# Performance work log

Hardware: AMD Instinct MI355X
Metric: run time of the kernel (lower is better)

Reference implementation:

```python
import jax, jax.numpy as jnp
import numpy as np

N_NODES = 100000
N_EDGES = 1600000
D_IN = 256
D_OUT = 128


def setup_inputs() -> dict:
    key = jax.random.key(0)
    k1, k2, k3, k4, k5, k6 = jax.random.split(key, 6)
    inp = {
        "input": jax.random.normal(k1, (N_NODES, D_IN), dtype=jnp.float32),
        "edge_row": jax.random.randint(k2, (N_EDGES,), 0, N_NODES),
        "edge_col": jax.random.randint(k3, (N_EDGES,), 0, N_NODES),
        "edge_val": jax.random.uniform(k4, (N_EDGES,), dtype=jnp.float32),
        "W": jax.random.normal(k5, (D_IN, D_OUT), dtype=jnp.float32) * (1.0 / np.sqrt(D_IN)),
        "b": jax.random.normal(k6, (D_OUT,), dtype=jnp.float32) * 0.01,
    }
    return inp


def reference(input, edge_row, edge_col, edge_val, W, b):
    # support = Linear(input)  -> [N, D_OUT]
    support = jnp.dot(input, W) + b
    # sparse.mm(adj, support): out[r] = sum_e val[e] * support[col[e]] for edges with row[e]==r
    msgs = edge_val[:, None] * support[edge_col]  # [E, D_OUT]
    agg = jax.ops.segment_sum(msgs, edge_row, num_segments=N_NODES)  # [N, D_OUT]
    return jnp.tanh(agg)
```

## Files before the change

kernel.cpp:

```cpp
#include <hip/hip_runtime.h>
#include <math.h>

#define N_NODES 100000
#define N_EDGES 1600000
#define D_IN 256
#define D_OUT 128

#define OFF_SUPPORT 0
#define OFF_COUNTS  51200000
#define OFF_CSREV   51600008
#define OFF_BSUMS   64400008
#define OFF_WTHI    64400416
#define OFF_WTLO    64465952

#define SCAN_CHUNK  1024
#define SCAN_BLOCKS ((N_NODES + SCAN_CHUNK - 1) / SCAN_CHUNK)

#define GB 128
#define GEMM_BLOCKS (((N_NODES + GB - 1) / GB) * 2)
#define EDGE_BLOCKS ((N_EDGES + 255) / 256)

typedef __attribute__((ext_vector_type(8))) short s8v;
typedef __attribute__((ext_vector_type(4))) float f4v;

__device__ __forceinline__ short f2bf(float x) {
  unsigned u = __float_as_uint(x);
  unsigned r = u + 0x7FFF + ((u >> 16) & 1);
  return (short)(r >> 16);
}
__device__ __forceinline__ float bf2f(short h) {
  return __uint_as_float(((unsigned)(unsigned short)h) << 16);
}

__device__ __forceinline__ void cvt8(float4 a, float4 b, s8v& h, s8v& l) {
  float f[8] = {a.x, a.y, a.z, a.w, b.x, b.y, b.z, b.w};
#pragma unroll
  for (int i = 0; i < 8; i++) {
    short hh = f2bf(f[i]);
    h[i] = hh;
    l[i] = f2bf(f[i] - bf2f(hh));
  }
}

typedef const float __attribute__((address_space(1)))* gas1f;
typedef float __attribute__((address_space(3)))* las3f;
__device__ __forceinline__ void gload_lds16(const float* g, float* l) {
  __builtin_amdgcn_global_load_lds((gas1f)g, (las3f)l, 16, 0, 0);
}

__global__ __launch_bounds__(256) void wconv_kernel(
    const float* __restrict__ W, short* __restrict__ wt_hi,
    short* __restrict__ wt_lo) {
  int idx = blockIdx.x * 256 + threadIdx.x;
  int k = idx >> 7;
  int n = idx & 127;
  float v = W[idx];
  short h = f2bf(v);
  wt_hi[n * 256 + k] = h;
  wt_lo[n * 256 + k] = f2bf(v - bf2f(h));
}

__device__ __forceinline__ void gemm_body(
    int gb, const float* __restrict__ input, const short* __restrict__ wt_hi,
    const short* __restrict__ wt_lo, const float* __restrict__ b,
    float* __restrict__ support) {
  __shared__ float Af[4][2][32][32];
  const int t = threadIdx.x;
  const int lane = t & 63;
  const int wv = t >> 6;
  const int qm = lane & 15;
  const int quad = lane >> 4;
  const int tile_m = gb >> 1;
  const int ch = gb & 1;
  const int node0 = tile_m * GB;
  const int col0 = ch * 64;

  const int srow = lane >> 3;
  const int gc = (lane & 7) ^ srow;

  auto stage = [&](int kt, int buf) {
#pragma unroll
    for (int j = 0; j < 4; ++j) {
      int nd = node0 + wv * 32 + j * 8 + srow;
      if (nd > N_NODES - 1) nd = N_NODES - 1;
      gload_lds16(input + (size_t)nd * D_IN + kt * 32 + gc * 4,
                  &Af[wv][buf][j * 8][0]);
    }
  };

  stage(0, 0);

  f4v acc[2][4];
#pragma unroll
  for (int mt = 0; mt < 2; mt++)
#pragma unroll
    for (int nt = 0; nt < 4; nt++) acc[mt][nt] = (f4v){0.f, 0.f, 0.f, 0.f};

  const int p0 = (2 * quad) ^ (qm & 7);
  const int p1 = (2 * quad + 1) ^ (qm & 7);

#pragma unroll
  for (int kt = 0; kt < 8; ++kt) {
    const int cb = kt & 1;
    asm volatile("s_waitcnt vmcnt(0)" ::: "memory");
    float4 x00 = *(const float4*)&Af[wv][cb][qm][p0 * 4];
    float4 x01 = *(const float4*)&Af[wv][cb][qm][p1 * 4];
    float4 x10 = *(const float4*)&Af[wv][cb][qm + 16][p0 * 4];
    float4 x11 = *(const float4*)&Af[wv][cb][qm + 16][p1 * 4];

    const int koff = kt * 32 + quad * 8;
    s8v bh[4], bl[4];
#pragma unroll
    for (int nt = 0; nt < 4; ++nt) {
      size_t bo = (size_t)(col0 + nt * 16 + qm) * 256 + koff;
      bh[nt] = *(const s8v*)(wt_hi + bo);
      bl[nt] = *(const s8v*)(wt_lo + bo);
    }
    __builtin_amdgcn_sched_barrier(0);
    if (kt < 7) stage(kt + 1, cb ^ 1);
    __builtin_amdgcn_sched_barrier(0);

    s8v ah0, al0, ah1, al1;
    cvt8(x00, x01, ah0, al0);
    cvt8(x10, x11, ah1, al1);
#pragma unroll
    for (int nt = 0; nt < 4; ++nt) {
      acc[0][nt] = __builtin_amdgcn_mfma_f32_16x16x32_bf16(ah0, bh[nt], acc[0][nt], 0, 0, 0);
      acc[0][nt] = __builtin_amdgcn_mfma_f32_16x16x32_bf16(ah0, bl[nt], acc[0][nt], 0, 0, 0);
      acc[0][nt] = __builtin_amdgcn_mfma_f32_16x16x32_bf16(al0, bh[nt], acc[0][nt], 0, 0, 0);
      acc[1][nt] = __builtin_amdgcn_mfma_f32_16x16x32_bf16(ah1, bh[nt], acc[1][nt], 0, 0, 0);
      acc[1][nt] = __builtin_amdgcn_mfma_f32_16x16x32_bf16(ah1, bl[nt], acc[1][nt], 0, 0, 0);
      acc[1][nt] = __builtin_amdgcn_mfma_f32_16x16x32_bf16(al1, bh[nt], acc[1][nt], 0, 0, 0);
    }
  }

  float bias[4];
#pragma unroll
  for (int nt = 0; nt < 4; nt++) bias[nt] = b[col0 + nt * 16 + qm];
#pragma unroll
  for (int mt = 0; mt < 2; mt++) {
#pragma unroll
    for (int nt = 0; nt < 4; nt++) {
      int col = col0 + nt * 16 + qm;
#pragma unroll
      for (int r = 0; r < 4; r++) {
        int node = node0 + wv * 32 + mt * 16 + quad * 4 + r;
        if (node < N_NODES)
          support[(size_t)node * D_OUT + col] = acc[mt][nt][r] + bias[nt];
      }
    }
  }
}

__global__ __launch_bounds__(256, 4) void gemm_hist_kernel(
    const float* __restrict__ input, const short* __restrict__ wt_hi,
    const short* __restrict__ wt_lo, const float* __restrict__ b,
    float* __restrict__ support, const int* __restrict__ erow,
    int* __restrict__ counts, int* __restrict__ pos_e) {
  if (blockIdx.x < GEMM_BLOCKS) {
    gemm_body(blockIdx.x, input, wt_hi, wt_lo, b, support);
  } else {
    int e = (blockIdx.x - GEMM_BLOCKS) * 256 + threadIdx.x;
    if (e < N_EDGES) pos_e[e] = atomicAdd(&counts[erow[e]], 1);
  }
}

__global__ __launch_bounds__(256) void build_kernel(
    const int* __restrict__ erow, const int* __restrict__ ecol,
    const float* __restrict__ eval, const int* __restrict__ offsets,
    const int* __restrict__ pos_e, int2* __restrict__ csr_ev) {
  int e = blockIdx.x * 256 + threadIdx.x;
  if (e < N_EDGES) {
    int idx = offsets[erow[e]] + pos_e[e];
    csr_ev[idx] = make_int2(ecol[e], __float_as_int(eval[e]));
  }
}

__global__ __launch_bounds__(256) void scan_phase1(const int* __restrict__ counts,
                                                   int* __restrict__ bsums) {
  __shared__ int ts[256];
  int t = threadIdx.x;
  int idx0 = blockIdx.x * SCAN_CHUNK + t * 4;
  int s = 0;
#pragma unroll
  for (int i = 0; i < 4; i++)
    if (idx0 + i < N_NODES) s += counts[idx0 + i];
  ts[t] = s;
  __syncthreads();
#pragma unroll
  for (int off = 128; off > 0; off >>= 1) {
    if (t < off) ts[t] += ts[t + off];
    __syncthreads();
  }
  if (t == 0) bsums[blockIdx.x] = ts[0];
}

__global__ __launch_bounds__(128) void scan_phase2(int* __restrict__ bsums) {
  __shared__ int s[128];
  int t = threadIdx.x;
  int v = (t < SCAN_BLOCKS) ? bsums[t] : 0;
  s[t] = v;
  __syncthreads();
#pragma unroll
  for (int off = 1; off < 128; off <<= 1) {
    int x = (t >= off) ? s[t - off] : 0;
    __syncthreads();
    s[t] += x;
    __syncthreads();
  }
  if (t < SCAN_BLOCKS) bsums[t] = s[t] - v;
}

__global__ __launch_bounds__(256) void scan_phase3(int* __restrict__ counts,
                                                   const int* __restrict__ bsums) {
  __shared__ int ts[256];
  int t = threadIdx.x;
  int b = blockIdx.x;
  int idx0 = b * SCAN_CHUNK + t * 4;
  int v[4];
  int s = 0;
#pragma unroll
  for (int i = 0; i < 4; i++) {
    v[i] = (idx0 + i < N_NODES) ? counts[idx0 + i] : 0;
    s += v[i];
  }
  ts[t] = s;
  __syncthreads();
#pragma unroll
  for (int off = 1; off < 256; off <<= 1) {
    int x = (t >= off) ? ts[t - off] : 0;
    __syncthreads();
    ts[t] += x;
    __syncthreads();
  }
  int run = bsums[b] + ts[t] - s;
#pragma unroll
  for (int i = 0; i < 4; i++) {
    int idx = idx0 + i;
    if (idx < N_NODES) counts[idx] = run;
    run += v[i];
  }
  if (b == 0 && t == 0) counts[N_NODES] = N_EDGES;
}

__global__ __launch_bounds__(256) void agg_kernel(
    const int* __restrict__ offsets, const int2* __restrict__ csr_ev,
    const float* __restrict__ support, float* __restrict__ out) {
  int r = blockIdx.x * 8 + (threadIdx.x >> 5);
  int l4 = (threadIdx.x & 31) * 4;
  int beg = offsets[r];
  int end = offsets[r + 1];
  float4 acc = make_float4(0.f, 0.f, 0.f, 0.f);
  int j = beg;
  for (; j + 8 <= end; j += 8) {
    int2 e[8];
    float4 s[8];
#pragma unroll
    for (int u = 0; u < 8; u++) e[u] = csr_ev[j + u];
#pragma unroll
    for (int u = 0; u < 8; u++)
      s[u] = *(const float4*)(support + (size_t)e[u].x * D_OUT + l4);
#pragma unroll
    for (int u = 0; u < 8; u++) {
      float v = __int_as_float(e[u].y);
      acc.x = fmaf(v, s[u].x, acc.x);
      acc.y = fmaf(v, s[u].y, acc.y);
      acc.z = fmaf(v, s[u].z, acc.z);
      acc.w = fmaf(v, s[u].w, acc.w);
    }
  }
  for (; j < end; j++) {
    int2 ev = csr_ev[j];
    float4 s = *(const float4*)(support + (size_t)ev.x * D_OUT + l4);
    float v = __int_as_float(ev.y);
    acc.x = fmaf(v, s.x, acc.x);
    acc.y = fmaf(v, s.y, acc.y);
    acc.z = fmaf(v, s.z, acc.z);
    acc.w = fmaf(v, s.w, acc.w);
  }
  *(float4*)(out + (size_t)r * D_OUT + l4) =
      make_float4(tanhf(acc.x), tanhf(acc.y), tanhf(acc.z), tanhf(acc.w));
}

extern "C" void kernel_launch(void* const* d_in, const int* in_sizes, int n_in,
                              void* d_out, int out_size, void* d_ws, size_t ws_size,
                              hipStream_t stream) {
  const float* input = (const float*)d_in[0];
  const int* erow = (const int*)d_in[1];
  const int* ecol = (const int*)d_in[2];
  const float* eval = (const float*)d_in[3];
  const float* W = (const float*)d_in[4];
  const float* b = (const float*)d_in[5];
  float* out = (float*)d_out;

  char* ws = (char*)d_ws;
  float* support = (float*)(ws + OFF_SUPPORT);
  int* counts = (int*)(ws + OFF_COUNTS);
  int2* csr_ev = (int2*)(ws + OFF_CSREV);
  int* bsums = (int*)(ws + OFF_BSUMS);
  short* wt_hi = (short*)(ws + OFF_WTHI);
  short* wt_lo = (short*)(ws + OFF_WTLO);
  int* pos_e = (int*)d_out;

  hipLaunchKernelGGL(wconv_kernel, dim3((D_IN * D_OUT) / 256), dim3(256), 0,
                     stream, W, wt_hi, wt_lo);
  hipMemsetAsync(ws + OFF_COUNTS, 0, (size_t)(N_NODES + 1) * 4, stream);

  hipLaunchKernelGGL(gemm_hist_kernel, dim3(GEMM_BLOCKS + EDGE_BLOCKS),
                     dim3(256), 0, stream, input, wt_hi, wt_lo, b, support,
                     erow, counts, pos_e);
  hipLaunchKernelGGL(scan_phase1, dim3(SCAN_BLOCKS), dim3(256), 0, stream,
                     counts, bsums);
  hipLaunchKernelGGL(scan_phase2, dim3(1), dim3(128), 0, stream, bsums);
  hipLaunchKernelGGL(scan_phase3, dim3(SCAN_BLOCKS), dim3(256), 0, stream,
                     counts, bsums);
  hipLaunchKernelGGL(build_kernel, dim3(EDGE_BLOCKS), dim3(256), 0, stream,
                     erow, ecol, eval, counts, pos_e, csr_ev);
  hipLaunchKernelGGL(agg_kernel, dim3(N_NODES / 8), dim3(256), 0, stream,
                     counts, csr_ev, support, out);
}
```

Measured before the change: 457.2 us.

## Split GEMM from histogram, widen GEMM tile to all columns, deepen prefetch

Each GEMM block now computes all 128 output columns for its 128 rows, so each input tile is read once instead of twice. The A-tile staging becomes two stages deep with a partial vmcnt wait, so loads stay in flight across iterations. The fused GEMM+histogram kernel is split into separate hist and gemm launches, which gives up the overlap of atomics with GEMM work. Doubling the accumulators and B registers raises register pressure, and launch bounds drop from 4 to 2 blocks per CU.

```diff
diff --git a/kernel.cpp b/kernel.cpp
--- a/kernel.cpp
+++ b/kernel.cpp
@@ -17,7 +17,7 @@
 #define SCAN_BLOCKS ((N_NODES + SCAN_CHUNK - 1) / SCAN_CHUNK)
 
 #define GB 128
-#define GEMM_BLOCKS (((N_NODES + GB - 1) / GB) * 2)
+#define GEMM_BLOCKS ((N_NODES + GB - 1) / GB)
 #define EDGE_BLOCKS ((N_EDGES + 255) / 256)
 
 typedef __attribute__((ext_vector_type(8))) short s8v;
@@ -60,20 +60,18 @@
   wt_lo[n * 256 + k] = f2bf(v - bf2f(h));
 }
 
-__device__ __forceinline__ void gemm_body(
-    int gb, const float* __restrict__ input, const short* __restrict__ wt_hi,
+__global__ __launch_bounds__(256, 2) void gemm_kernel(
+    const float* __restrict__ input, const short* __restrict__ wt_hi,
     const short* __restrict__ wt_lo, const float* __restrict__ b,
     float* __restrict__ support) {
   __shared__ float Af[4][2][32][32];
+  const int gb = blockIdx.x;
   const int t = threadIdx.x;
   const int lane = t & 63;
   const int wv = t >> 6;
   const int qm = lane & 15;
   const int quad = lane >> 4;
-  const int tile_m = gb >> 1;
-  const int ch = gb & 1;
-  const int node0 = tile_m * GB;
-  const int col0 = ch * 64;
+  const int node0 = gb * GB;
 
   const int srow = lane >> 3;
   const int gc = (lane & 7) ^ srow;
@@ -89,12 +87,13 @@
   };
 
   stage(0, 0);
-
-  f4v acc[2][4];
+  stage(1, 1);
+
+  f4v acc[2][8];
 #pragma unroll
   for (int mt = 0; mt < 2; mt++)
 #pragma unroll
-    for (int nt = 0; nt < 4; nt++) acc[mt][nt] = (f4v){0.f, 0.f, 0.f, 0.f};
+    for (int nt = 0; nt < 8; nt++) acc[mt][nt] = (f4v){0.f, 0.f, 0.f, 0.f};
 
   const int p0 = (2 * quad) ^ (qm & 7);
   const int p1 = (2 * quad + 1) ^ (qm & 7);
@@ -102,29 +101,31 @@
 #pragma unroll
   for (int kt = 0; kt < 8; ++kt) {
     const int cb = kt & 1;
-    asm volatile("s_waitcnt vmcnt(0)" ::: "memory");
+    asm volatile("s_waitcnt vmcnt(4)" ::: "memory");
     float4 x00 = *(const float4*)&Af[wv][cb][qm][p0 * 4];
     float4 x01 = *(const float4*)&Af[wv][cb][qm][p1 * 4];
     float4 x10 = *(const float4*)&Af[wv][cb][qm + 16][p0 * 4];
     float4 x11 = *(const float4*)&Af[wv][cb][qm + 16][p1 * 4];
+    asm volatile("s_waitcnt lgkmcnt(0)" ::: "memory");
+    __builtin_amdgcn_sched_barrier(0);
 
     const int koff = kt * 32 + quad * 8;
-    s8v bh[4], bl[4];
-#pragma unroll
-    for (int nt = 0; nt < 4; ++nt) {
-      size_t bo = (size_t)(col0 + nt * 16 + qm) * 256 + koff;
+    s8v bh[8], bl[8];
+#pragma unroll
+    for (int nt = 0; nt < 8; ++nt) {
+      size_t bo = (size_t)(nt * 16 + qm) * 256 + koff;
       bh[nt] = *(const s8v*)(wt_hi + bo);
       bl[nt] = *(const s8v*)(wt_lo + bo);
     }
     __builtin_amdgcn_sched_barrier(0);
-    if (kt < 7) stage(kt + 1, cb ^ 1);
+    if (kt < 6) stage(kt + 2, cb);
     __builtin_amdgcn_sched_barrier(0);
 
     s8v ah0, al0, ah1, al1;
     cvt8(x00, x01, ah0, al0);
     cvt8(x10, x11, ah1, al1);
 #pragma unroll
-    for (int nt = 0; nt < 4; ++nt) {
+    for (int nt = 0; nt < 8; ++nt) {
       acc[0][nt] = __builtin_amdgcn_mfma_f32_16x16x32_bf16(ah0, bh[nt], acc[0][nt], 0, 0, 0);
       acc[0][nt] = __builtin_amdgcn_mfma_f32_16x16x32_bf16(ah0, bl[nt], acc[0][nt], 0, 0, 0);
       acc[0][nt] = __builtin_amdgcn_mfma_f32_16x16x32_bf16(al0, bh[nt], acc[0][nt], 0, 0, 0);
@@ -134,14 +135,14 @@
     }
   }
 
-  float bias[4];
-#pragma unroll
-  for (int nt = 0; nt < 4; nt++) bias[nt] = b[col0 + nt * 16 + qm];
+  float bias[8];
+#pragma unroll
+  for (int nt = 0; nt < 8; nt++) bias[nt] = b[nt * 16 + qm];
 #pragma unroll
   for (int mt = 0; mt < 2; mt++) {
 #pragma unroll
-    for (int nt = 0; nt < 4; nt++) {
-      int col = col0 + nt * 16 + qm;
+    for (int nt = 0; nt < 8; nt++) {
+      int col = nt * 16 + qm;
 #pragma unroll
       for (int r = 0; r < 4; r++) {
         int node = node0 + wv * 32 + mt * 16 + quad * 4 + r;
@@ -152,17 +153,11 @@
   }
 }
 
-__global__ __launch_bounds__(256, 4) void gemm_hist_kernel(
-    const float* __restrict__ input, const short* __restrict__ wt_hi,
-    const short* __restrict__ wt_lo, const float* __restrict__ b,
-    float* __restrict__ support, const int* __restrict__ erow,
-    int* __restrict__ counts, int* __restrict__ pos_e) {
-  if (blockIdx.x < GEMM_BLOCKS) {
-    gemm_body(blockIdx.x, input, wt_hi, wt_lo, b, support);
-  } else {
-    int e = (blockIdx.x - GEMM_BLOCKS) * 256 + threadIdx.x;
-    if (e < N_EDGES) pos_e[e] = atomicAdd(&counts[erow[e]], 1);
-  }
+__global__ __launch_bounds__(256) void hist_kernel(
+    const int* __restrict__ erow, int* __restrict__ counts,
+    int* __restrict__ pos_e) {
+  int e = blockIdx.x * 256 + threadIdx.x;
+  if (e < N_EDGES) pos_e[e] = atomicAdd(&counts[erow[e]], 1);
 }
 
 __global__ __launch_bounds__(256) void build_kernel(
@@ -306,9 +301,10 @@
                      stream, W, wt_hi, wt_lo);
   hipMemsetAsync(ws + OFF_COUNTS, 0, (size_t)(N_NODES + 1) * 4, stream);
 
-  hipLaunchKernelGGL(gemm_hist_kernel, dim3(GEMM_BLOCKS + EDGE_BLOCKS),
-                     dim3(256), 0, stream, input, wt_hi, wt_lo, b, support,
+  hipLaunchKernelGGL(hist_kernel, dim3(EDGE_BLOCKS), dim3(256), 0, stream,
                      erow, counts, pos_e);
+  hipLaunchKernelGGL(gemm_kernel, dim3(GEMM_BLOCKS), dim3(256), 0, stream,
+                     input, wt_hi, wt_lo, b, support);
   hipLaunchKernelGGL(scan_phase1, dim3(SCAN_BLOCKS), dim3(256), 0, stream,
                      counts, bsums);
   hipLaunchKernelGGL(scan_phase2, dim3(1), dim3(128), 0, stream, bsums);
```

After: 475.7 us. +4.0%, slower.
